# Kernel optimization log

Measured on AMD Instinct MI355X. Metric: run time of the kernel, lower is better.

Reference implementation:

```python
import jax, jax.numpy as jnp
import numpy as np

N = 100000
E = 1250000
D = 64
G = 256  # num graphs
OUT = 2
BN_EPS = 1e-5


def setup_inputs() -> dict:
    key = jax.random.key(0)
    ks = jax.random.split(key, 32)
    def lin(k, fi, fo):
        return jax.random.normal(k, (fi, fo), jnp.float32) / np.sqrt(fi)
    inp = {
        "x": jax.random.normal(ks[0], (N, D), jnp.float32),
        "edge_index": jax.random.randint(ks[1], (2, E), 0, N, jnp.int32),
        "batch": jnp.sort(jax.random.randint(ks[2], (N,), 0, G, jnp.int32)),
        "w0a": lin(ks[3], D, D), "b0a": jax.random.normal(ks[4], (D,)) * 0.02,
        "w0b": lin(ks[5], D, D), "b0b": jax.random.normal(ks[6], (D,)) * 0.02,
        "w1a": lin(ks[7], D, D), "b1a": jax.random.normal(ks[8], (D,)) * 0.02,
        "w1b": lin(ks[9], D, D), "b1b": jax.random.normal(ks[10], (D,)) * 0.02,
        "w2a": lin(ks[11], D, D), "b2a": jax.random.normal(ks[12], (D,)) * 0.02,
        "w2b": lin(ks[13], D, D), "b2b": jax.random.normal(ks[14], (D,)) * 0.02,
        "bn0_g": jax.random.uniform(ks[15], (D,), minval=0.5, maxval=1.5),
        "bn0_b": jax.random.normal(ks[16], (D,)) * 0.02,
        "bn0_m": jax.random.normal(ks[17], (D,)) * 0.1,
        "bn0_v": jax.random.uniform(ks[18], (D,), minval=0.5, maxval=1.5),
        "bn1_g": jax.random.uniform(ks[19], (D,), minval=0.5, maxval=1.5),
        "bn1_b": jax.random.normal(ks[20], (D,)) * 0.02,
        "bn1_m": jax.random.normal(ks[21], (D,)) * 0.1,
        "bn1_v": jax.random.uniform(ks[22], (D,), minval=0.5, maxval=1.5),
        "wp1": lin(ks[23], 2 * D, D), "bp1": jax.random.normal(ks[24], (D,)) * 0.02,
        "wp2": lin(ks[25], D, OUT), "bp2": jax.random.normal(ks[26], (OUT,)) * 0.02,
    }
    return inp


def _gin(x, edge_index, wa, ba, wb, bb):
    # GINConv (eps=0): MLP(x + sum_{j->i} x_j); messages flow src->dst
    agg = jax.ops.segment_sum(x[edge_index[0]], edge_index[1], num_segments=N)
    h = x + agg
    h = jnp.maximum(h @ wa + ba, 0.0) @ wb + bb
    return h


def _bn(x, g, b, m, v):
    return (x - m) * (g * jax.lax.rsqrt(v + BN_EPS)) + b


def reference(x, edge_index, batch,
              w0a, b0a, w0b, b0b, w1a, b1a, w1b, b1b, w2a, b2a, w2b, b2b,
              bn0_g, bn0_b, bn0_m, bn0_v, bn1_g, bn1_b, bn1_m, bn1_v,
              wp1, bp1, wp2, bp2):
    # eval mode: dropout = identity, BatchNorm uses running stats
    h = jnp.maximum(_gin(x, edge_index, w0a, b0a, w0b, b0b), 0.0)
    h = _bn(h, bn0_g, bn0_b, bn0_m, bn0_v)
    h = jnp.maximum(_gin(h, edge_index, w1a, b1a, w1b, b1b), 0.0)
    h = _bn(h, bn1_g, bn1_b, bn1_m, bn1_v)
    h = jnp.maximum(_gin(h, edge_index, w2a, b2a, w2b, b2b), 0.0)
    # global mean + max pool over graphs
    counts = jax.ops.segment_sum(jnp.ones((N,), h.dtype), batch, num_segments=G)
    mean = jax.ops.segment_sum(h, batch, num_segments=G) / jnp.maximum(counts, 1.0)[:, None]
    mx = jax.ops.segment_max(h, batch, num_segments=G)
    mx = jnp.where(jnp.isfinite(mx), mx, 0.0)  # guard empty graphs
    graph_x = jnp.concatenate([mean, mx], axis=1)  # [G, 2D]
    pred = (graph_x @ wp1 + bp1) @ wp2 + bp2
    return jax.nn.log_softmax(pred, axis=1)
```

## Files before the change

kernel.cpp:

```cpp
#include <hip/hip_runtime.h>
#include <hip/hip_bf16.h>

#define NN 100000
#define EE 1250000
#define DD 64
#define GG 256
#define COARSE 1024
#define NC ((NN + COARSE - 1) / COARSE)
#define CHUNK 2048
#define NCHUNK ((EE + CHUNK - 1) / CHUNK)

static __device__ __forceinline__ float relu_f(float x) { return fmaxf(x, 0.0f); }

static __device__ __forceinline__ float b2f(ushort u) {
    return __uint_as_float(((unsigned int)u) << 16);
}
static __device__ __forceinline__ ushort f2b(float f) {
    __hip_bfloat16 h = __float2bfloat16(f);
    return *(ushort*)&h;
}

__global__ __launch_bounds__(256) void hist2_kernel(const int* __restrict__ dst,
                                                    int* __restrict__ ghist, int E) {
    __shared__ int h[NC];
    int t = threadIdx.x;
    if (t < NC) h[t] = 0;
    __syncthreads();
    for (int e = blockIdx.x * blockDim.x + t; e < E; e += gridDim.x * blockDim.x)
        atomicAdd(&h[dst[e] >> 10], 1);
    __syncthreads();
    if (t < NC && h[t]) atomicAdd(&ghist[t], h[t]);
}

__global__ void scan2_kernel(const int* __restrict__ ghist, int* __restrict__ coffs,
                             int* __restrict__ gcursor) {
    if (threadIdx.x == 0) {
        int run = 0;
        for (int b = 0; b < NC; b++) {
            coffs[b] = run;
            gcursor[b] = run;
            run += ghist[b];
        }
        coffs[NC] = run;
    }
}

__global__ __launch_bounds__(256) void bin_kernel(
    const int* __restrict__ ei, int* __restrict__ gcursor, int* __restrict__ epack, int E) {
    __shared__ int hist[NC];
    __shared__ int base[NC];
    __shared__ int lpre[NC];
    __shared__ int scnt;
    __shared__ int lbuf[CHUNK];
    __shared__ int lobuf[CHUNK];
    int t = threadIdx.x;
    for (int c = blockIdx.x; c < NCHUNK; c += gridDim.x) {
        int e0 = c * CHUNK;
        if (t < NC) hist[t] = 0;
        __syncthreads();
        int myb[8], myloc[8], mypack[8];
#pragma unroll
        for (int q = 0; q < 8; q++) {
            int e = e0 + q * 256 + t;
            if (e < E) {
                int d = ei[E + e];
                int s = ei[e];
                int b = d >> 10;
                myb[q] = b;
                mypack[q] = s | ((d & (COARSE - 1)) << 17);
                myloc[q] = atomicAdd(&hist[b], 1);
            } else myb[q] = -1;
        }
        __syncthreads();
        if (t < NC) base[t] = hist[t] ? atomicAdd(&gcursor[t], hist[t]) : 0;
        if (t == 0) {
            int run = 0;
            for (int b = 0; b < NC; b++) { lpre[b] = run; run += hist[b]; }
            scnt = run;
        }
        __syncthreads();
#pragma unroll
        for (int q = 0; q < 8; q++) {
            if (myb[q] >= 0) {
                int p = lpre[myb[q]] + myloc[q];
                lbuf[p] = mypack[q];
                lobuf[p] = base[myb[q]] + myloc[q];
            }
        }
        __syncthreads();
        int cnt = scnt;
#pragma unroll
        for (int q = 0; q < 8; q++) {
            int p = q * 256 + t;
            if (p < cnt) epack[lobuf[p]] = lbuf[p];
        }
        __syncthreads();
    }
}

__global__ __launch_bounds__(256) void csr2_kernel(
    const int* __restrict__ epack, const int* __restrict__ coffs,
    int* __restrict__ srcs, int* __restrict__ off) {
    __shared__ int hist[COARSE];
    __shared__ int tmp[256];
    int b = blockIdx.x;
    int t = threadIdx.x;
    int c0 = coffs[b], c1 = coffs[b + 1];
    int nbase = b * COARSE;
#pragma unroll
    for (int j = 0; j < 4; j++) hist[t * 4 + j] = 0;
    __syncthreads();
    for (int e = c0 + t; e < c1; e += 256)
        atomicAdd(&hist[epack[e] >> 17], 1);
    __syncthreads();
    int h0 = hist[t * 4], h1 = hist[t * 4 + 1], h2 = hist[t * 4 + 2], h3 = hist[t * 4 + 3];
    int s4 = h0 + h1 + h2 + h3;
    tmp[t] = s4;
    __syncthreads();
    for (int d = 1; d < 256; d <<= 1) {
        int v = (t >= d) ? tmp[t - d] : 0;
        __syncthreads();
        tmp[t] += v;
        __syncthreads();
    }
    int run = tmp[t] - s4;
    int pre0 = run; run += h0;
    int pre1 = run; run += h1;
    int pre2 = run; run += h2;
    int pre3 = run;
    int pres[4] = {pre0, pre1, pre2, pre3};
#pragma unroll
    for (int j = 0; j < 4; j++) {
        int node = nbase + t * 4 + j;
        if (node < NN) off[node] = c0 + pres[j];
        hist[t * 4 + j] = pres[j];
    }
    if (b == NC - 1 && t == 0) off[NN] = c1;
    __syncthreads();
    for (int e = c0 + t; e < c1; e += 256) {
        int p = epack[e];
        int pos = c0 + atomicAdd(&hist[p >> 17], 1);
        srcs[pos] = p & 0x1FFFF;
    }
}

__global__ void bounds_kernel(const int* __restrict__ batch, int* __restrict__ gstart, int n) {
    int i = blockIdx.x * blockDim.x + threadIdx.x;
    if (i >= n) return;
    int b = batch[i];
    int prev = (i == 0) ? -1 : batch[i - 1];
    for (int g = prev + 1; g <= b; g++) gstart[g] = i;
    if (i == n - 1) {
        for (int g = b + 1; g <= GG; g++) gstart[g] = n;
    }
}

__global__ __launch_bounds__(256) void cast_kernel(const float* __restrict__ x,
                                                   ushort* __restrict__ xb) {
    size_t i = ((size_t)blockIdx.x * blockDim.x + threadIdx.x) * 4;
    if (i >= (size_t)NN * DD) return;
    float4 v = *(const float4*)(x + i);
    ushort4 r;
    r.x = f2b(v.x); r.y = f2b(v.y); r.z = f2b(v.z); r.w = f2b(v.w);
    *(ushort4*)(xb + i) = r;
}

__global__ __launch_bounds__(256) void agg_kernel(
    const ushort* __restrict__ xb, float* __restrict__ u,
    const int* __restrict__ off, const int* __restrict__ srcs, int n) {
    int node = blockIdx.x * 4 + (threadIdx.x >> 6);
    int lane = threadIdx.x & 63;
    if (node >= n) return;
    int o = off[node];
    int oe = off[node + 1];
    float a0 = b2f(xb[(size_t)node * DD + lane]);
    float a1 = 0.0f, a2 = 0.0f, a3 = 0.0f, a4 = 0.0f, a5 = 0.0f, a6 = 0.0f, a7 = 0.0f;
    int j = o;
    for (; j + 8 <= oe; j += 8) {
        int s0 = srcs[j + 0], s1 = srcs[j + 1], s2 = srcs[j + 2], s3 = srcs[j + 3];
        int s4 = srcs[j + 4], s5 = srcs[j + 5], s6 = srcs[j + 6], s7 = srcs[j + 7];
        ushort v0 = xb[(size_t)s0 * DD + lane];
        ushort v1 = xb[(size_t)s1 * DD + lane];
        ushort v2 = xb[(size_t)s2 * DD + lane];
        ushort v3 = xb[(size_t)s3 * DD + lane];
        ushort v4 = xb[(size_t)s4 * DD + lane];
        ushort v5 = xb[(size_t)s5 * DD + lane];
        ushort v6 = xb[(size_t)s6 * DD + lane];
        ushort v7 = xb[(size_t)s7 * DD + lane];
        a0 += b2f(v0); a1 += b2f(v1); a2 += b2f(v2); a3 += b2f(v3);
        a4 += b2f(v4); a5 += b2f(v5); a6 += b2f(v6); a7 += b2f(v7);
    }
    for (; j + 4 <= oe; j += 4) {
        int s0 = srcs[j + 0], s1 = srcs[j + 1], s2 = srcs[j + 2], s3 = srcs[j + 3];
        ushort v0 = xb[(size_t)s0 * DD + lane];
        ushort v1 = xb[(size_t)s1 * DD + lane];
        ushort v2 = xb[(size_t)s2 * DD + lane];
        ushort v3 = xb[(size_t)s3 * DD + lane];
        a0 += b2f(v0); a1 += b2f(v1); a2 += b2f(v2); a3 += b2f(v3);
    }
    for (; j < oe; j++) a0 += b2f(xb[(size_t)srcs[j] * DD + lane]);
    u[(size_t)node * DD + lane] = ((a0 + a1) + (a2 + a3)) + ((a4 + a5) + (a6 + a7));
}

template <bool HAS_BN, bool OUT_BF16>
__global__ __launch_bounds__(256) void mlp_kernel(
    const float* __restrict__ u, void* __restrict__ hout,
    const float* __restrict__ wa, const float* __restrict__ ba,
    const float* __restrict__ wb, const float* __restrict__ bb,
    const float* __restrict__ bng, const float* __restrict__ bnb,
    const float* __restrict__ bnm, const float* __restrict__ bnv, int n) {
    __shared__ float At[DD][68];
    __shared__ float Wt[DD * DD];
    int t = threadIdx.x;
    int r0 = blockIdx.x * DD;
    int tx = t & 15, ty = t >> 4;
    int i0 = tx * 4, j0 = ty * 4;

    {
        int ii = t >> 2;
        int cb = (t & 3) * 16;
        int row = r0 + ii;
        if (row < n) {
            const float4* ur = (const float4*)(u + (size_t)row * DD + cb);
            float4 v0 = ur[0], v1 = ur[1], v2 = ur[2], v3 = ur[3];
            At[cb + 0][ii] = v0.x;  At[cb + 1][ii] = v0.y;
            At[cb + 2][ii] = v0.z;  At[cb + 3][ii] = v0.w;
            At[cb + 4][ii] = v1.x;  At[cb + 5][ii] = v1.y;
            At[cb + 6][ii] = v1.z;  At[cb + 7][ii] = v1.w;
            At[cb + 8][ii] = v2.x;  At[cb + 9][ii] = v2.y;
            At[cb + 10][ii] = v2.z; At[cb + 11][ii] = v2.w;
            At[cb + 12][ii] = v3.x; At[cb + 13][ii] = v3.y;
            At[cb + 14][ii] = v3.z; At[cb + 15][ii] = v3.w;
        } else {
#pragma unroll
            for (int q = 0; q < 16; q++) At[cb + q][ii] = 0.0f;
        }
#pragma unroll
        for (int rep = 0; rep < 4; rep++) {
            int idx = rep * 1024 + t * 4;
            *(float4*)&Wt[idx] = *(const float4*)&wa[idx];
        }
    }
    __syncthreads();

    float acc[4][4];
#pragma unroll
    for (int a = 0; a < 4; a++)
#pragma unroll
        for (int b = 0; b < 4; b++) acc[a][b] = 0.0f;
#pragma unroll 4
    for (int k = 0; k < DD; k++) {
        float4 av = *(const float4*)&At[k][i0];
        float4 wv = *(const float4*)&Wt[k * DD + j0];
        float aa[4] = {av.x, av.y, av.z, av.w};
        float ww[4] = {wv.x, wv.y, wv.z, wv.w};
#pragma unroll
        for (int di = 0; di < 4; di++)
#pragma unroll
            for (int dj = 0; dj < 4; dj++)
                acc[di][dj] = fmaf(aa[di], ww[dj], acc[di][dj]);
    }
    float4 ba4 = *(const float4*)&ba[j0];
    float bav[4] = {ba4.x, ba4.y, ba4.z, ba4.w};
    __syncthreads();

#pragma unroll
    for (int dj = 0; dj < 4; dj++) {
        float4 w;
        w.x = relu_f(acc[0][dj] + bav[dj]);
        w.y = relu_f(acc[1][dj] + bav[dj]);
        w.z = relu_f(acc[2][dj] + bav[dj]);
        w.w = relu_f(acc[3][dj] + bav[dj]);
        *(float4*)&At[j0 + dj][i0] = w;
    }
#pragma unroll
    for (int rep = 0; rep < 4; rep++) {
        int idx = rep * 1024 + t * 4;
        *(float4*)&Wt[idx] = *(const float4*)&wb[idx];
    }
    __syncthreads();

    float acc2[4][4];
#pragma unroll
    for (int a = 0; a < 4; a++)
#pragma unroll
        for (int b = 0; b < 4; b++) acc2[a][b] = 0.0f;
#pragma unroll 4
    for (int k = 0; k < DD; k++) {
        float4 av = *(const float4*)&At[k][i0];
        float4 wv = *(const float4*)&Wt[k * DD + j0];
        float aa[4] = {av.x, av.y, av.z, av.w};
        float ww[4] = {wv.x, wv.y, wv.z, wv.w};
#pragma unroll
        for (int di = 0; di < 4; di++)
#pragma unroll
            for (int dj = 0; dj < 4; dj++)
                acc2[di][dj] = fmaf(aa[di], ww[dj], acc2[di][dj]);
    }

    float4 bb4 = *(const float4*)&bb[j0];
    float bbv[4] = {bb4.x, bb4.y, bb4.z, bb4.w};
    float scv[4] = {0, 0, 0, 0}, shv[4] = {0, 0, 0, 0};
    if (HAS_BN) {
        float4 g4 = *(const float4*)&bng[j0];
        float4 b4 = *(const float4*)&bnb[j0];
        float4 m4 = *(const float4*)&bnm[j0];
        float4 v4 = *(const float4*)&bnv[j0];
        float gg[4] = {g4.x, g4.y, g4.z, g4.w};
        float bbn[4] = {b4.x, b4.y, b4.z, b4.w};
        float mm[4] = {m4.x, m4.y, m4.z, m4.w};
        float vv[4] = {v4.x, v4.y, v4.z, v4.w};
#pragma unroll
        for (int c = 0; c < 4; c++) {
            scv[c] = gg[c] * rsqrtf(vv[c] + 1e-5f);
            shv[c] = bbn[c] - mm[c] * scv[c];
        }
    }
#pragma unroll
    for (int di = 0; di < 4; di++) {
        int row = r0 + i0 + di;
        if (row >= n) break;
        float v[4];
#pragma unroll
        for (int dj = 0; dj < 4; dj++) {
            float tv = relu_f(acc2[di][dj] + bbv[dj]);
            if (HAS_BN) tv = fmaf(tv, scv[dj], shv[dj]);
            v[dj] = tv;
        }
        if (OUT_BF16) {
            ushort4 r;
            r.x = f2b(v[0]); r.y = f2b(v[1]); r.z = f2b(v[2]); r.w = f2b(v[3]);
            *(ushort4*)((ushort*)hout + (size_t)row * DD + j0) = r;
        } else {
            float4 r; r.x = v[0]; r.y = v[1]; r.z = v[2]; r.w = v[3];
            *(float4*)((float*)hout + (size_t)row * DD + j0) = r;
        }
    }
}

__global__ __launch_bounds__(256) void poolhead_kernel(
    const float* __restrict__ h, const int* __restrict__ gstart,
    const float* __restrict__ wp1, const float* __restrict__ bp1,
    const float* __restrict__ wp2, const float* __restrict__ bp2,
    float* __restrict__ out) {
    __shared__ float ssum[4][DD];
    __shared__ float smax[4][DD];
    __shared__ float gx[2 * DD];
    int g = blockIdx.x;
    int lane = threadIdx.x & 63;
    int wave = threadIdx.x >> 6;
    int s = gstart[g], e = gstart[g + 1];
    float sum = 0.0f, mx = 0.0f;
    for (int i = s + wave; i < e; i += 4) {
        float v = h[(size_t)i * DD + lane];
        sum += v;
        mx = fmaxf(mx, v);
    }
    ssum[wave][lane] = sum;
    smax[wave][lane] = mx;
    __syncthreads();
    if (wave == 0) {
        sum = ssum[0][lane] + ssum[1][lane] + ssum[2][lane] + ssum[3][lane];
        mx = fmaxf(fmaxf(smax[0][lane], smax[1][lane]),
                   fmaxf(smax[2][lane], smax[3][lane]));
        float cnt = fmaxf((float)(e - s), 1.0f);
        gx[lane] = sum / cnt;
        gx[DD + lane] = mx;
    }
    __syncthreads();
    if (wave == 0) {
        float tt = bp1[lane];
        for (int k = 0; k < 2 * DD; k++) tt = fmaf(gx[k], wp1[k * DD + lane], tt);
        float p0 = tt * wp2[lane * 2 + 0];
        float p1 = tt * wp2[lane * 2 + 1];
        for (int o = 32; o > 0; o >>= 1) {
            p0 += __shfl_down(p0, o);
            p1 += __shfl_down(p1, o);
        }
        if (lane == 0) {
            p0 += bp2[0];
            p1 += bp2[1];
            float m = fmaxf(p0, p1);
            float lse = m + logf(expf(p0 - m) + expf(p1 - m));
            out[g * 2 + 0] = p0 - lse;
            out[g * 2 + 1] = p1 - lse;
        }
    }
}

extern "C" void kernel_launch(void* const* d_in, const int* in_sizes, int n_in,
                              void* d_out, int out_size, void* d_ws, size_t ws_size,
                              hipStream_t stream) {
    const float* x     = (const float*)d_in[0];
    const int*   ei    = (const int*)d_in[1];
    const int*   batch = (const int*)d_in[2];
    const float* w0a = (const float*)d_in[3];  const float* b0a = (const float*)d_in[4];
    const float* w0b = (const float*)d_in[5];  const float* b0b = (const float*)d_in[6];
    const float* w1a = (const float*)d_in[7];  const float* b1a = (const float*)d_in[8];
    const float* w1b = (const float*)d_in[9];  const float* b1b = (const float*)d_in[10];
    const float* w2a = (const float*)d_in[11]; const float* b2a = (const float*)d_in[12];
    const float* w2b = (const float*)d_in[13]; const float* b2b = (const float*)d_in[14];
    const float* bn0g = (const float*)d_in[15]; const float* bn0b = (const float*)d_in[16];
    const float* bn0m = (const float*)d_in[17]; const float* bn0v = (const float*)d_in[18];
    const float* bn1g = (const float*)d_in[19]; const float* bn1b = (const float*)d_in[20];
    const float* bn1m = (const float*)d_in[21]; const float* bn1v = (const float*)d_in[22];
    const float* wp1 = (const float*)d_in[23]; const float* bp1 = (const float*)d_in[24];
    const float* wp2 = (const float*)d_in[25]; const float* bp2 = (const float*)d_in[26];
    float* out = (float*)d_out;

    char* p = (char*)d_ws;
    auto take = [&](size_t bytes) {
        char* r = p;
        p += (bytes + 255) & ~(size_t)255;
        return r;
    };
    int* ghist   = (int*)take(NC * sizeof(int));
    int* coffs   = (int*)take((NC + 1) * sizeof(int));
    int* gcursor = (int*)take(NC * sizeof(int));
    int* epack   = (int*)take(EE * sizeof(int));
    int* srcs    = (int*)take(EE * sizeof(int));
    int* off     = (int*)take((NN + 1) * sizeof(int));
    int* gstart  = (int*)take((GG + 1) * sizeof(int));
    ushort* xb   = (ushort*)take((size_t)NN * DD * sizeof(ushort));
    float* bufU  = (float*)take((size_t)NN * DD * sizeof(float));
    ushort* hA   = (ushort*)take((size_t)NN * DD * sizeof(ushort));
    ushort* hB   = (ushort*)take((size_t)NN * DD * sizeof(ushort));
    float* hC    = (float*)take((size_t)NN * DD * sizeof(float));

    hipMemsetAsync(ghist, 0, NC * sizeof(int), stream);
    hist2_kernel<<<512, 256, 0, stream>>>(ei + EE, ghist, EE);
    scan2_kernel<<<1, 64, 0, stream>>>(ghist, coffs, gcursor);
    bin_kernel<<<512, 256, 0, stream>>>(ei, gcursor, epack, EE);
    csr2_kernel<<<NC, 256, 0, stream>>>(epack, coffs, srcs, off);
    bounds_kernel<<<(NN + 255) / 256, 256, 0, stream>>>(batch, gstart, NN);
    cast_kernel<<<(NN * DD / 4 + 255) / 256, 256, 0, stream>>>(x, xb);

    int agg_grid = (NN + 3) / 4;
    int mlp_grid = (NN + DD - 1) / DD;

    agg_kernel<<<agg_grid, 256, 0, stream>>>(xb, bufU, off, srcs, NN);
    mlp_kernel<true, true><<<mlp_grid, 256, 0, stream>>>(bufU, hA, w0a, b0a, w0b, b0b,
                                                         bn0g, bn0b, bn0m, bn0v, NN);
    agg_kernel<<<agg_grid, 256, 0, stream>>>(hA, bufU, off, srcs, NN);
    mlp_kernel<true, true><<<mlp_grid, 256, 0, stream>>>(bufU, hB, w1a, b1a, w1b, b1b,
                                                         bn1g, bn1b, bn1m, bn1v, NN);
    agg_kernel<<<agg_grid, 256, 0, stream>>>(hB, bufU, off, srcs, NN);
    mlp_kernel<false, false><<<mlp_grid, 256, 0, stream>>>(bufU, hC, w2a, b2a, w2b, b2b,
                                                           nullptr, nullptr, nullptr, nullptr, NN);

    poolhead_kernel<<<GG, 256, 0, stream>>>(hC, gstart, wp1, bp1, wp2, bp2, out);
}
```

Before: 341.3 us.

## Run GIN MLP GEMMs on MFMA using split-bf16 hi/lo emulation

Replaces the fp32 FMA-based two-layer MLP with MFMA 16x16x32 bf16 instructions. Both activations and weights are split into high and low bf16 parts, and three MFMAs (hi*hi, lo*hi, hi*lo) recover near-fp32 accuracy. A new prep kernel transposes and splits the six weight matrices once per call. This is meant to cut the ALU-bound GEMM cost in the three MLP kernels. In exchange it adds conversion work, an extra launch, and per-element scattered output stores.

```diff
diff --git a/kernel.cpp b/kernel.cpp
--- a/kernel.cpp
+++ b/kernel.cpp
@@ -9,6 +9,10 @@
 #define NC ((NN + COARSE - 1) / COARSE)
 #define CHUNK 2048
 #define NCHUNK ((EE + CHUNK - 1) / CHUNK)
+#define PAD 72
+
+typedef short bf8_t __attribute__((ext_vector_type(8)));
+typedef float f4_t __attribute__((ext_vector_type(4)));
 
 static __device__ __forceinline__ float relu_f(float x) { return fmaxf(x, 0.0f); }
 
@@ -163,6 +167,31 @@
     ushort4 r;
     r.x = f2b(v.x); r.y = f2b(v.y); r.z = f2b(v.z); r.w = f2b(v.w);
     *(ushort4*)(xb + i) = r;
+}
+
+__global__ __launch_bounds__(256) void prepw_kernel(
+    const float* __restrict__ w0a, const float* __restrict__ w0b,
+    const float* __restrict__ w1a, const float* __restrict__ w1b,
+    const float* __restrict__ w2a, const float* __restrict__ w2b,
+    ushort* __restrict__ wt) {
+    const float* srcs_[6] = {w0a, w0b, w1a, w1b, w2a, w2b};
+    const float* src = srcs_[blockIdx.x];
+    ushort* dhi = wt + (size_t)(2 * blockIdx.x) * DD * DD;
+    ushort* dlo = wt + (size_t)(2 * blockIdx.x + 1) * DD * DD;
+    int t = threadIdx.x;
+    int nn = t >> 2, kseg = (t & 3) * 16;
+    ushort thi[16], tlo[16];
+#pragma unroll
+    for (int q = 0; q < 16; q++) {
+        float v = src[(size_t)(kseg + q) * DD + nn];
+        ushort hh = f2b(v);
+        thi[q] = hh;
+        tlo[q] = f2b(v - b2f(hh));
+    }
+    *(uint4*)&dhi[nn * DD + kseg] = *(uint4*)&thi[0];
+    *(uint4*)&dhi[nn * DD + kseg + 8] = *(uint4*)&thi[8];
+    *(uint4*)&dlo[nn * DD + kseg] = *(uint4*)&tlo[0];
+    *(uint4*)&dlo[nn * DD + kseg + 8] = *(uint4*)&tlo[8];
 }
 
 __global__ __launch_bounds__(256) void agg_kernel(
@@ -203,137 +232,131 @@
 }
 
 template <bool HAS_BN, bool OUT_BF16>
-__global__ __launch_bounds__(256) void mlp_kernel(
+__global__ __launch_bounds__(256) void mlpm_kernel(
     const float* __restrict__ u, void* __restrict__ hout,
-    const float* __restrict__ wa, const float* __restrict__ ba,
-    const float* __restrict__ wb, const float* __restrict__ bb,
+    const ushort* __restrict__ wah, const ushort* __restrict__ wal,
+    const float* __restrict__ ba,
+    const ushort* __restrict__ wbh, const ushort* __restrict__ wbl,
+    const float* __restrict__ bb,
     const float* __restrict__ bng, const float* __restrict__ bnb,
     const float* __restrict__ bnm, const float* __restrict__ bnv, int n) {
-    __shared__ float At[DD][68];
-    __shared__ float Wt[DD * DD];
+    __shared__ ushort Ahi[DD][PAD];
+    __shared__ ushort Alo[DD][PAD];
+    __shared__ ushort Wh[DD][PAD];
+    __shared__ ushort Wl[DD][PAD];
     int t = threadIdx.x;
     int r0 = blockIdx.x * DD;
-    int tx = t & 15, ty = t >> 4;
-    int i0 = tx * 4, j0 = ty * 4;
+    int w = t >> 6, l = t & 63;
+    int lr = l & 15, lg = l >> 4;
+    int srow = t >> 2, sseg = t & 3;
 
     {
-        int ii = t >> 2;
-        int cb = (t & 3) * 16;
-        int row = r0 + ii;
-        if (row < n) {
-            const float4* ur = (const float4*)(u + (size_t)row * DD + cb);
-            float4 v0 = ur[0], v1 = ur[1], v2 = ur[2], v3 = ur[3];
-            At[cb + 0][ii] = v0.x;  At[cb + 1][ii] = v0.y;
-            At[cb + 2][ii] = v0.z;  At[cb + 3][ii] = v0.w;
-            At[cb + 4][ii] = v1.x;  At[cb + 5][ii] = v1.y;
-            At[cb + 6][ii] = v1.z;  At[cb + 7][ii] = v1.w;
-            At[cb + 8][ii] = v2.x;  At[cb + 9][ii] = v2.y;
-            At[cb + 10][ii] = v2.z; At[cb + 11][ii] = v2.w;
-            At[cb + 12][ii] = v3.x; At[cb + 13][ii] = v3.y;
-            At[cb + 14][ii] = v3.z; At[cb + 15][ii] = v3.w;
+        int grow = r0 + srow;
+        ushort thi[16], tlo[16];
+        if (grow < n) {
+            const float4* up = (const float4*)(u + (size_t)grow * DD + sseg * 16);
+#pragma unroll
+            for (int q = 0; q < 4; q++) {
+                float4 v = up[q];
+                float vv[4] = {v.x, v.y, v.z, v.w};
+#pragma unroll
+                for (int c = 0; c < 4; c++) {
+                    ushort hh = f2b(vv[c]);
+                    thi[q * 4 + c] = hh;
+                    tlo[q * 4 + c] = f2b(vv[c] - b2f(hh));
+                }
+            }
         } else {
 #pragma unroll
-            for (int q = 0; q < 16; q++) At[cb + q][ii] = 0.0f;
-        }
-#pragma unroll
-        for (int rep = 0; rep < 4; rep++) {
-            int idx = rep * 1024 + t * 4;
-            *(float4*)&Wt[idx] = *(const float4*)&wa[idx];
-        }
-    }
-    __syncthreads();
-
-    float acc[4][4];
-#pragma unroll
-    for (int a = 0; a < 4; a++)
-#pragma unroll
-        for (int b = 0; b < 4; b++) acc[a][b] = 0.0f;
-#pragma unroll 4
-    for (int k = 0; k < DD; k++) {
-        float4 av = *(const float4*)&At[k][i0];
-        float4 wv = *(const float4*)&Wt[k * DD + j0];
-        float aa[4] = {av.x, av.y, av.z, av.w};
-        float ww[4] = {wv.x, wv.y, wv.z, wv.w};
-#pragma unroll
-        for (int di = 0; di < 4; di++)
-#pragma unroll
-            for (int dj = 0; dj < 4; dj++)
-                acc[di][dj] = fmaf(aa[di], ww[dj], acc[di][dj]);
-    }
-    float4 ba4 = *(const float4*)&ba[j0];
-    float bav[4] = {ba4.x, ba4.y, ba4.z, ba4.w};
-    __syncthreads();
-
-#pragma unroll
-    for (int dj = 0; dj < 4; dj++) {
-        float4 w;
-        w.x = relu_f(acc[0][dj] + bav[dj]);
-        w.y = relu_f(acc[1][dj] + bav[dj]);
-        w.z = relu_f(acc[2][dj] + bav[dj]);
-        w.w = relu_f(acc[3][dj] + bav[dj]);
-        *(float4*)&At[j0 + dj][i0] = w;
-    }
-#pragma unroll
-    for (int rep = 0; rep < 4; rep++) {
-        int idx = rep * 1024 + t * 4;
-        *(float4*)&Wt[idx] = *(const float4*)&wb[idx];
-    }
-    __syncthreads();
-
-    float acc2[4][4];
-#pragma unroll
-    for (int a = 0; a < 4; a++)
-#pragma unroll
-        for (int b = 0; b < 4; b++) acc2[a][b] = 0.0f;
-#pragma unroll 4
-    for (int k = 0; k < DD; k++) {
-        float4 av = *(const float4*)&At[k][i0];
-        float4 wv = *(const float4*)&Wt[k * DD + j0];
-        float aa[4] = {av.x, av.y, av.z, av.w};
-        float ww[4] = {wv.x, wv.y, wv.z, wv.w};
-#pragma unroll
-        for (int di = 0; di < 4; di++)
-#pragma unroll
-            for (int dj = 0; dj < 4; dj++)
-                acc2[di][dj] = fmaf(aa[di], ww[dj], acc2[di][dj]);
-    }
-
-    float4 bb4 = *(const float4*)&bb[j0];
-    float bbv[4] = {bb4.x, bb4.y, bb4.z, bb4.w};
-    float scv[4] = {0, 0, 0, 0}, shv[4] = {0, 0, 0, 0};
-    if (HAS_BN) {
-        float4 g4 = *(const float4*)&bng[j0];
-        float4 b4 = *(const float4*)&bnb[j0];
-        float4 m4 = *(const float4*)&bnm[j0];
-        float4 v4 = *(const float4*)&bnv[j0];
-        float gg[4] = {g4.x, g4.y, g4.z, g4.w};
-        float bbn[4] = {b4.x, b4.y, b4.z, b4.w};
-        float mm[4] = {m4.x, m4.y, m4.z, m4.w};
-        float vv[4] = {v4.x, v4.y, v4.z, v4.w};
-#pragma unroll
-        for (int c = 0; c < 4; c++) {
-            scv[c] = gg[c] * rsqrtf(vv[c] + 1e-5f);
-            shv[c] = bbn[c] - mm[c] * scv[c];
-        }
-    }
-#pragma unroll
-    for (int di = 0; di < 4; di++) {
-        int row = r0 + i0 + di;
-        if (row >= n) break;
-        float v[4];
-#pragma unroll
-        for (int dj = 0; dj < 4; dj++) {
-            float tv = relu_f(acc2[di][dj] + bbv[dj]);
-            if (HAS_BN) tv = fmaf(tv, scv[dj], shv[dj]);
-            v[dj] = tv;
-        }
-        if (OUT_BF16) {
-            ushort4 r;
-            r.x = f2b(v[0]); r.y = f2b(v[1]); r.z = f2b(v[2]); r.w = f2b(v[3]);
-            *(ushort4*)((ushort*)hout + (size_t)row * DD + j0) = r;
-        } else {
-            float4 r; r.x = v[0]; r.y = v[1]; r.z = v[2]; r.w = v[3];
-            *(float4*)((float*)hout + (size_t)row * DD + j0) = r;
+            for (int q = 0; q < 16; q++) { thi[q] = 0; tlo[q] = 0; }
+        }
+        *(uint4*)&Ahi[srow][sseg * 16] = *(uint4*)&thi[0];
+        *(uint4*)&Ahi[srow][sseg * 16 + 8] = *(uint4*)&thi[8];
+        *(uint4*)&Alo[srow][sseg * 16] = *(uint4*)&tlo[0];
+        *(uint4*)&Alo[srow][sseg * 16 + 8] = *(uint4*)&tlo[8];
+        const uint4* whp = (const uint4*)(wah + srow * DD + sseg * 16);
+        *(uint4*)&Wh[srow][sseg * 16] = whp[0];
+        *(uint4*)&Wh[srow][sseg * 16 + 8] = whp[1];
+        const uint4* wlp = (const uint4*)(wal + srow * DD + sseg * 16);
+        *(uint4*)&Wl[srow][sseg * 16] = wlp[0];
+        *(uint4*)&Wl[srow][sseg * 16 + 8] = wlp[1];
+    }
+    __syncthreads();
+
+    f4_t acc[4];
+#pragma unroll
+    for (int nt = 0; nt < 4; nt++) acc[nt] = (f4_t){0.0f, 0.0f, 0.0f, 0.0f};
+#pragma unroll
+    for (int ks = 0; ks < 2; ks++) {
+        bf8_t ah = *(const bf8_t*)&Ahi[w * 16 + lr][ks * 32 + lg * 8];
+        bf8_t al = *(const bf8_t*)&Alo[w * 16 + lr][ks * 32 + lg * 8];
+#pragma unroll
+        for (int nt = 0; nt < 4; nt++) {
+            bf8_t bh = *(const bf8_t*)&Wh[nt * 16 + lr][ks * 32 + lg * 8];
+            bf8_t bl = *(const bf8_t*)&Wl[nt * 16 + lr][ks * 32 + lg * 8];
+            acc[nt] = __builtin_amdgcn_mfma_f32_16x16x32_bf16(ah, bh, acc[nt], 0, 0, 0);
+            acc[nt] = __builtin_amdgcn_mfma_f32_16x16x32_bf16(al, bh, acc[nt], 0, 0, 0);
+            acc[nt] = __builtin_amdgcn_mfma_f32_16x16x32_bf16(ah, bl, acc[nt], 0, 0, 0);
+        }
+    }
+#pragma unroll
+    for (int nt = 0; nt < 4; nt++) {
+        float bav = ba[nt * 16 + lr];
+#pragma unroll
+        for (int r = 0; r < 4; r++) {
+            float z = relu_f(acc[nt][r] + bav);
+            ushort zh = f2b(z);
+            Ahi[w * 16 + lg * 4 + r][nt * 16 + lr] = zh;
+            Alo[w * 16 + lg * 4 + r][nt * 16 + lr] = f2b(z - b2f(zh));
+        }
+    }
+    __syncthreads();
+
+    {
+        const uint4* whp = (const uint4*)(wbh + srow * DD + sseg * 16);
+        *(uint4*)&Wh[srow][sseg * 16] = whp[0];
+        *(uint4*)&Wh[srow][sseg * 16 + 8] = whp[1];
+        const uint4* wlp = (const uint4*)(wbl + srow * DD + sseg * 16);
+        *(uint4*)&Wl[srow][sseg * 16] = wlp[0];
+        *(uint4*)&Wl[srow][sseg * 16 + 8] = wlp[1];
+    }
+    __syncthreads();
+
+    f4_t acc2[4];
+#pragma unroll
+    for (int nt = 0; nt < 4; nt++) acc2[nt] = (f4_t){0.0f, 0.0f, 0.0f, 0.0f};
+#pragma unroll
+    for (int ks = 0; ks < 2; ks++) {
+        bf8_t ah = *(const bf8_t*)&Ahi[w * 16 + lr][ks * 32 + lg * 8];
+        bf8_t al = *(const bf8_t*)&Alo[w * 16 + lr][ks * 32 + lg * 8];
+#pragma unroll
+        for (int nt = 0; nt < 4; nt++) {
+            bf8_t bh = *(const bf8_t*)&Wh[nt * 16 + lr][ks * 32 + lg * 8];
+            bf8_t bl = *(const bf8_t*)&Wl[nt * 16 + lr][ks * 32 + lg * 8];
+            acc2[nt] = __builtin_amdgcn_mfma_f32_16x16x32_bf16(ah, bh, acc2[nt], 0, 0, 0);
+            acc2[nt] = __builtin_amdgcn_mfma_f32_16x16x32_bf16(al, bh, acc2[nt], 0, 0, 0);
+            acc2[nt] = __builtin_amdgcn_mfma_f32_16x16x32_bf16(ah, bl, acc2[nt], 0, 0, 0);
+        }
+    }
+
+#pragma unroll
+    for (int nt = 0; nt < 4; nt++) {
+        int col = nt * 16 + lr;
+        float bbv = bb[col];
+        float sc = 1.0f, sh = 0.0f;
+        if (HAS_BN) {
+            sc = bng[col] * rsqrtf(bnv[col] + 1e-5f);
+            sh = bnb[col] - bnm[col] * sc;
+        }
+#pragma unroll
+        for (int r = 0; r < 4; r++) {
+            int row = r0 + w * 16 + lg * 4 + r;
+            if (row < n) {
+                float v = relu_f(acc2[nt][r] + bbv);
+                if (HAS_BN) v = fmaf(v, sc, sh);
+                if (OUT_BF16) ((ushort*)hout)[(size_t)row * DD + col] = f2b(v);
+                else ((float*)hout)[(size_t)row * DD + col] = v;
+            }
         }
     }
 }
@@ -426,6 +449,7 @@
     ushort* hA   = (ushort*)take((size_t)NN * DD * sizeof(ushort));
     ushort* hB   = (ushort*)take((size_t)NN * DD * sizeof(ushort));
     float* hC    = (float*)take((size_t)NN * DD * sizeof(float));
+    ushort* wt   = (ushort*)take(12 * DD * DD * sizeof(ushort));
 
     hipMemsetAsync(ghist, 0, NC * sizeof(int), stream);
     hist2_kernel<<<512, 256, 0, stream>>>(ei + EE, ghist, EE);
@@ -434,19 +458,27 @@
     csr2_kernel<<<NC, 256, 0, stream>>>(epack, coffs, srcs, off);
     bounds_kernel<<<(NN + 255) / 256, 256, 0, stream>>>(batch, gstart, NN);
     cast_kernel<<<(NN * DD / 4 + 255) / 256, 256, 0, stream>>>(x, xb);
+    prepw_kernel<<<6, 256, 0, stream>>>(w0a, w0b, w1a, w1b, w2a, w2b, wt);
 
     int agg_grid = (NN + 3) / 4;
     int mlp_grid = (NN + DD - 1) / DD;
+    const size_t M = (size_t)DD * DD;
+    ushort* w0ah = wt + 0 * M;  ushort* w0al = wt + 1 * M;
+    ushort* w0bh = wt + 2 * M;  ushort* w0bl = wt + 3 * M;
+    ushort* w1ah = wt + 4 * M;  ushort* w1al = wt + 5 * M;
+    ushort* w1bh = wt + 6 * M;  ushort* w1bl = wt + 7 * M;
+    ushort* w2ah = wt + 8 * M;  ushort* w2al = wt + 9 * M;
+    ushort* w2bh = wt + 10 * M; ushort* w2bl = wt + 11 * M;
 
     agg_kernel<<<agg_grid, 256, 0, stream>>>(xb, bufU, off, srcs, NN);
-    mlp_kernel<true, true><<<mlp_grid, 256, 0, stream>>>(bufU, hA, w0a, b0a, w0b, b0b,
-                                                         bn0g, bn0b, bn0m, bn0v, NN);
+    mlpm_kernel<true, true><<<mlp_grid, 256, 0, stream>>>(
+        bufU, hA, w0ah, w0al, b0a, w0bh, w0bl, b0b, bn0g, bn0b, bn0m, bn0v, NN);
     agg_kernel<<<agg_grid, 256, 0, stream>>>(hA, bufU, off, srcs, NN);
-    mlp_kernel<true, true><<<mlp_grid, 256, 0, stream>>>(bufU, hB, w1a, b1a, w1b, b1b,
-                                                         bn1g, bn1b, bn1m, bn1v, NN);
+    mlpm_kernel<true, true><<<mlp_grid, 256, 0, stream>>>(
+        bufU, hB, w1ah, w1al, b1a, w1bh, w1bl, b1b, bn1g, bn1b, bn1m, bn1v, NN);
     agg_kernel<<<agg_grid, 256, 0, stream>>>(hB, bufU, off, srcs, NN);
-    mlp_kernel<false, false><<<mlp_grid, 256, 0, stream>>>(bufU, hC, w2a, b2a, w2b, b2b,
-                                                           nullptr, nullptr, nullptr, nullptr, NN);
+    mlpm_kernel<false, false><<<mlp_grid, 256, 0, stream>>>(
+        bufU, hC, w2ah, w2al, b2a, w2bh, w2bl, b2b, nullptr, nullptr, nullptr, nullptr, NN);
 
     poolhead_kernel<<<GG, 256, 0, stream>>>(hC, gstart, wp1, bp1, wp2, bp2, out);
 }
```

After: 310.1 us. 9.2% less time.
